# Kernel optimization log

Hardware: AMD Instinct MI355X
Metric: run time of the kernel (lower is better)

The kernel has to match this reference:

```python
import jax, jax.numpy as jnp
import numpy as np

NEG_SLOPE = 0.2
LN_EPS = 1e-5


def gat_conv(x, edge_index, W, att_src, att_dst, bias, heads, out_ch, concat):
    """PyG-style GATConv with add_self_loops=True, eval mode (no dropout)."""
    N = x.shape[0]
    loop = jnp.arange(N, dtype=edge_index.dtype)
    src = jnp.concatenate([edge_index[0], loop])
    dst = jnp.concatenate([edge_index[1], loop])
    h = (x @ W).reshape(N, heads, out_ch)                      # [N,H,C]
    a_src = jnp.sum(h * att_src, axis=-1)                      # [N,H]
    a_dst = jnp.sum(h * att_dst, axis=-1)                      # [N,H]
    e = jax.nn.leaky_relu(a_src[src] + a_dst[dst], NEG_SLOPE)  # [E,H]
    emax = jax.ops.segment_max(e, dst, num_segments=N)         # [N,H]
    ex = jnp.exp(e - emax[dst])
    denom = jax.ops.segment_sum(ex, dst, num_segments=N)       # [N,H]
    alpha = ex / denom[dst]                                    # [E,H]
    msg = h[src] * alpha[..., None]                            # [E,H,C]
    out = jax.ops.segment_sum(msg, dst, num_segments=N)        # [N,H,C]
    out = out.reshape(N, heads * out_ch) if concat else out.mean(axis=1)
    return out + bias


def layer_norm(x, w, b):
    mu = x.mean(-1, keepdims=True)
    var = jnp.mean((x - mu) ** 2, -1, keepdims=True)
    return (x - mu) * jax.lax.rsqrt(var + LN_EPS) * w + b


def setup_inputs() -> dict:
    key = jax.random.key(0)
    ks = jax.random.split(key, 16)
    N, E, R = 50000, 800000, 16
    node_dim, res_dim, hidden, heads = 128, 64, 64, 2
    s = lambda fan: 1.0 / np.sqrt(fan)
    return {
        "x": jax.random.normal(ks[0], (N, node_dim), jnp.float32),
        "edge_index": jax.random.randint(ks[1], (2, E), 0, N, jnp.int64),
        "resource_features": jax.random.normal(ks[2], (N, R, res_dim), jnp.float32),
        "W1": jax.random.normal(ks[3], (node_dim, heads * hidden), jnp.float32) * s(node_dim),
        "att_src1": jax.random.normal(ks[4], (heads, hidden), jnp.float32) * s(hidden),
        "att_dst1": jax.random.normal(ks[5], (heads, hidden), jnp.float32) * s(hidden),
        "b1": jnp.zeros((heads * hidden,), jnp.float32),
        "W2": jax.random.normal(ks[6], (heads * hidden, hidden), jnp.float32) * s(heads * hidden),
        "att_src2": jax.random.normal(ks[7], (1, hidden), jnp.float32) * s(hidden),
        "att_dst2": jax.random.normal(ks[8], (1, hidden), jnp.float32) * s(hidden),
        "b2": jnp.zeros((hidden,), jnp.float32),
        "ln_w": jnp.ones((hidden,), jnp.float32),
        "ln_b": jnp.zeros((hidden,), jnp.float32),
        "res_W": jax.random.normal(ks[9], (res_dim, hidden), jnp.float32) * s(res_dim),
        "res_b": jnp.zeros((hidden,), jnp.float32),
    }


def reference(x, edge_index, resource_features, W1, att_src1, att_dst1, b1,
              W2, att_src2, att_dst2, b2, ln_w, ln_b, res_W, res_b):
    hidden = W2.shape[1]
    heads = att_src1.shape[0]
    h = jax.nn.elu(gat_conv(x, edge_index, W1, att_src1, att_dst1, b1,
                            heads, hidden, concat=True))
    h = gat_conv(h, edge_index, W2, att_src2, att_dst2, b2,
                 1, hidden, concat=False)
    h = layer_norm(h, ln_w, ln_b)                              # [N, hidden]
    R = resource_features.shape[1]
    x_expanded = jnp.broadcast_to(h[:, None, :], (h.shape[0], R, hidden))
    res_emb = jax.nn.elu(resource_features @ res_W + res_b)    # [N,R,hidden]
    return jnp.concatenate([x_expanded, res_emb], axis=-1)     # [N,R,2*hidden]
```

## Files before the change

kernel.cpp:

```cpp
#include <hip/hip_runtime.h>
#include <hip/hip_bf16.h>
#include <math.h>

#define LEAKY_SLOPE 0.2f
#define LN_EPS 1e-5f

typedef __attribute__((ext_vector_type(4))) float f32x4;
typedef __attribute__((ext_vector_type(8))) short short8;

__device__ __forceinline__ float leaky_relu(float x) { return x >= 0.f ? x : LEAKY_SLOPE * x; }
__device__ __forceinline__ float elu1(float x) { return x > 0.f ? x : expm1f(x); }
__device__ __forceinline__ short f2bf(float f) {
    union { __hip_bfloat16 b; short s; } u;
    u.b = __float2bfloat16(f);
    return u.s;
}
__device__ __forceinline__ float bflo(unsigned u) { union { unsigned i; float f; } x; x.i = u << 16; return x.f; }
__device__ __forceinline__ float bfhi(unsigned u) { union { unsigned i; float f; } x; x.i = u & 0xffff0000u; return x.f; }
__device__ __forceinline__ float sbf(short s) { union { unsigned i; float f; } x; x.i = ((unsigned)(unsigned short)s) << 16; return x.f; }
__device__ __forceinline__ unsigned fkey(float f) {
    unsigned b = __float_as_uint(f);
    return b ^ (unsigned)(((int)b >> 31) | 0x80000000);
}
__device__ __forceinline__ float funkey(unsigned k) {
    unsigned b = (k & 0x80000000u) ? (k ^ 0x80000000u) : ~k;
    return __uint_as_float(b);
}

#define SUBW1 130
__global__ __launch_bounds__(256) void k_gemm1m(
    const float* __restrict__ x, const float* __restrict__ W1,
    const float* __restrict__ att_s, const float* __restrict__ att_d,
    short* __restrict__ h1, float* __restrict__ a_src, float* __restrict__ a_dst,
    unsigned* __restrict__ amax, int N)
{
    __shared__ short WT[16 * SUBW1 * 8];
    __shared__ float sb[64 * 4];
    __shared__ float wm[8];
    const int t = threadIdx.x;
    const int w = t >> 6, l = t & 63, lr = l & 15, lk = l >> 4;
    const int n0 = blockIdx.x * 64;
    for (int idx = t; idx < 16384; idx += 256) {
        int k = idx >> 7, col = idx & 127;
        WT[((k >> 3) * SUBW1 + col) * 8 + (k & 7)] = f2bf(W1[idx]);
    }
    sb[t] = 0.f;
    __syncthreads();

    f32x4 acc[4][2];
    #pragma unroll
    for (int mt = 0; mt < 4; ++mt)
        #pragma unroll
        for (int nt = 0; nt < 2; ++nt) acc[mt][nt] = (f32x4){0.f, 0.f, 0.f, 0.f};

    #pragma unroll
    for (int ks = 0; ks < 4; ++ks) {
        short8 bfr[2];
        #pragma unroll
        for (int nt = 0; nt < 2; ++nt) {
            int col = w * 32 + nt * 16 + lr;
            int kk = ks * 4 + lk;
            bfr[nt] = *(const short8*)&WT[(kk * SUBW1 + col) * 8];
        }
        #pragma unroll
        for (int mt = 0; mt < 4; ++mt) {
            int row = n0 + mt * 16 + lr; if (row >= N) row = N - 1;
            const float* ap = x + (size_t)row * 128 + ks * 32 + lk * 8;
            float4 u0 = *(const float4*)ap;
            float4 u1 = *(const float4*)(ap + 4);
            short8 af;
            af[0] = f2bf(u0.x); af[1] = f2bf(u0.y); af[2] = f2bf(u0.z); af[3] = f2bf(u0.w);
            af[4] = f2bf(u1.x); af[5] = f2bf(u1.y); af[6] = f2bf(u1.z); af[7] = f2bf(u1.w);
            acc[mt][0] = __builtin_amdgcn_mfma_f32_16x16x32_bf16(af, bfr[0], acc[mt][0], 0, 0, 0);
            acc[mt][1] = __builtin_amdgcn_mfma_f32_16x16x32_bf16(af, bfr[1], acc[mt][1], 0, 0, 0);
        }
    }

    const int head = w >> 1;
    float asv[2], adv[2];
    #pragma unroll
    for (int nt = 0; nt < 2; ++nt) {
        int ci = (w & 1) * 32 + nt * 16 + lr;
        asv[nt] = att_s[head * 64 + ci];
        adv[nt] = att_d[head * 64 + ci];
    }
    #pragma unroll
    for (int mt = 0; mt < 4; ++mt) {
        #pragma unroll
        for (int i = 0; i < 4; ++i) {
            float ps = acc[mt][0][i] * asv[0] + acc[mt][1][i] * asv[1];
            float pd = acc[mt][0][i] * adv[0] + acc[mt][1][i] * adv[1];
            #pragma unroll
            for (int o = 1; o < 16; o <<= 1) { ps += __shfl_xor(ps, o); pd += __shfl_xor(pd, o); }
            int rl = mt * 16 + lk * 4 + i;
            if (lr == 0) {
                atomicAdd(&sb[rl * 4 + head], ps);
                atomicAdd(&sb[rl * 4 + 2 + head], pd);
            }
            int row = n0 + rl;
            if (row < N) {
                h1[(size_t)row * 128 + w * 32 + lr]      = f2bf(acc[mt][0][i]);
                h1[(size_t)row * 128 + w * 32 + 16 + lr] = f2bf(acc[mt][1][i]);
            }
        }
    }
    __syncthreads();
    int nl = t >> 2, q = t & 3, n = n0 + nl;
    float v = sb[t];
    bool ok = (n < N);
    if (ok) {
        if (q == 0) a_src[n * 2 + 0] = v;
        else if (q == 1) a_src[n * 2 + 1] = v;
        else if (q == 2) a_dst[n * 2 + 0] = v;
        else a_dst[n * 2 + 1] = v;
    }
    float m0 = (ok && q == 0) ? v : -1e30f;
    float m1 = (ok && q == 1) ? v : -1e30f;
    #pragma unroll
    for (int o = 32; o; o >>= 1) { m0 = fmaxf(m0, __shfl_xor(m0, o)); m1 = fmaxf(m1, __shfl_xor(m1, o)); }
    if (l == 0) { wm[w] = m0; wm[4 + w] = m1; }
    __syncthreads();
    if (t == 0) {
        float M0 = fmaxf(fmaxf(wm[0], wm[1]), fmaxf(wm[2], wm[3]));
        float M1 = fmaxf(fmaxf(wm[4], wm[5]), fmaxf(wm[6], wm[7]));
        atomicMax(&amax[0], fkey(M0));
        atomicMax(&amax[1], fkey(M1));
    }
}

#define DETECT_IS64(ei, E)                                              \
    __shared__ int s_is64;                                              \
    {                                                                   \
        if (threadIdx.x < 64) {                                         \
            int v = (threadIdx.x < (E)) ? ((const int*)(ei))[2 * threadIdx.x + 1] : 0; \
            unsigned long long b = __ballot(v != 0);                    \
            if (threadIdx.x == 0) s_is64 = (b == 0ULL);                 \
        }                                                               \
        __syncthreads();                                                \
    }

__global__ __launch_bounds__(256) void k_deg(const void* __restrict__ ei, int E, int* __restrict__ deg)
{
    DETECT_IS64(ei, E)
    const int is64 = s_is64;
    for (int e = blockIdx.x * blockDim.x + threadIdx.x; e < E; e += gridDim.x * blockDim.x) {
        int d = is64 ? (int)((const long long*)ei)[(size_t)E + e] : ((const int*)ei)[(size_t)E + e];
        atomicAdd(&deg[d], 1);
    }
}

__global__ __launch_bounds__(256) void k_bsum(const int* __restrict__ deg, int* __restrict__ bsum, int n)
{
    __shared__ int ws[4];
    const int base = blockIdx.x * 1024;
    int s = 0;
    for (int j = threadIdx.x; j < 1024; j += 256) {
        int i = base + j;
        s += (i < n) ? deg[i] : 0;
    }
    #pragma unroll
    for (int o = 32; o; o >>= 1) s += __shfl_down(s, o);
    if ((threadIdx.x & 63) == 0) ws[threadIdx.x >> 6] = s;
    __syncthreads();
    if (threadIdx.x == 0) bsum[blockIdx.x] = ws[0] + ws[1] + ws[2] + ws[3];
}

__global__ void k_scanb(const int* __restrict__ bsum, int* __restrict__ bbase, int nb)
{
    const int l = threadIdx.x;
    int carry = 0;
    for (int b = 0; b < nb; b += 64) {
        int v = (b + l < nb) ? bsum[b + l] : 0;
        int x = v;
        #pragma unroll
        for (int o = 1; o < 64; o <<= 1) { int y = __shfl_up(x, o); if (l >= o) x += y; }
        if (b + l < nb) bbase[b + l] = carry + x - v;
        carry += __shfl(x, 63);
    }
}

__global__ __launch_bounds__(1024) void k_scan3(const int* __restrict__ deg, const int* __restrict__ bbase,
                                                int* __restrict__ offs, int* __restrict__ cursor, int n)
{
    __shared__ int ws[16];
    const int i = blockIdx.x * 1024 + threadIdx.x;
    const int l = threadIdx.x & 63, w = threadIdx.x >> 6;
    int v = (i < n) ? deg[i] : 0;
    int x = v;
    #pragma unroll
    for (int o = 1; o < 64; o <<= 1) { int y = __shfl_up(x, o); if (l >= o) x += y; }
    if (l == 63) ws[w] = x;
    __syncthreads();
    if (threadIdx.x < 16) {
        int s = ws[threadIdx.x];
        #pragma unroll
        for (int o = 1; o < 16; o <<= 1) { int y = __shfl_up(s, o); if (threadIdx.x >= o) s += y; }
        ws[threadIdx.x] = s;
    }
    __syncthreads();
    int add = (w ? ws[w - 1] : 0) + bbase[blockIdx.x];
    if (i < n) {
        offs[i + 1] = x + add;
        cursor[i] = x + add - v;
    }
    if (blockIdx.x == 0 && threadIdx.x == 0) offs[0] = 0;
}

__global__ __launch_bounds__(256) void k_scatter(const void* __restrict__ ei, int E,
                                                 int* __restrict__ cursor, int* __restrict__ csr_src)
{
    DETECT_IS64(ei, E)
    const int is64 = s_is64;
    for (int e = blockIdx.x * blockDim.x + threadIdx.x; e < E; e += gridDim.x * blockDim.x) {
        int s, d;
        if (is64) {
            const long long* p = (const long long*)ei;
            s = (int)p[e]; d = (int)p[(size_t)E + e];
        } else {
            const int* p = (const int*)ei;
            s = p[e]; d = p[(size_t)E + e];
        }
        int pos = atomicAdd(&cursor[d], 1);
        csr_src[pos] = s;
    }
}

__global__ __launch_bounds__(256) void k_layer1(
    const short* __restrict__ h1, const float* __restrict__ a_s, const float* __restrict__ a_d,
    const int* __restrict__ offs, const int* __restrict__ csr,
    const float* __restrict__ b1, const unsigned* __restrict__ amax,
    short* __restrict__ h1a, int N)
{
    const int w = threadIdx.x >> 6, l = threadIdx.x & 63;
    const int n = blockIdx.x * 4 + w;
    if (n >= N) return;
    const float2 adp = *(const float2*)&a_d[2 * n];
    const float2 asp = *(const float2*)&a_s[2 * n];
    const float C0 = leaky_relu(funkey(amax[0]) + adp.x);
    const float C1 = leaky_relu(funkey(amax[1]) + adp.y);
    const float es0 = leaky_relu(asp.x + adp.x) - C0;
    const float es1 = leaky_relu(asp.y + adp.y) - C1;
    const int hsel = l >> 5;
    const int o0 = offs[n], o1 = offs[n + 1];

    float den0 = 0.f, den1 = 0.f;
    float acc0 = 0.f, acc1 = 0.f, acc0b = 0.f, acc1b = 0.f;
    for (int base = o0; base < o1; base += 64) {
        const int cnt = min(64, o1 - base);
        int sidx = 0; float p0 = 0.f, p1 = 0.f;
        if (l < cnt) {
            sidx = csr[base + l];
            float2 av = *(const float2*)&a_s[2 * sidx];
            p0 = __expf(leaky_relu(av.x + adp.x) - C0);
            p1 = __expf(leaky_relu(av.y + adp.y) - C1);
        }
        den0 += p0; den1 += p1;
        int j = 0;
        for (; j + 2 <= cnt; j += 2) {
            int sa  = __shfl(sidx, j),     sb2 = __shfl(sidx, j + 1);
            float pa0 = __shfl(p0, j),     pb0 = __shfl(p0, j + 1);
            float pa1 = __shfl(p1, j),     pb1 = __shfl(p1, j + 1);
            unsigned ua = *(const unsigned*)(h1 + (size_t)sa  * 128 + 2 * l);
            unsigned ub = *(const unsigned*)(h1 + (size_t)sb2 * 128 + 2 * l);
            float pa = hsel ? pa1 : pa0, pb = hsel ? pb1 : pb0;
            acc0  += pa * bflo(ua); acc1  += pa * bfhi(ua);
            acc0b += pb * bflo(ub); acc1b += pb * bfhi(ub);
        }
        if (j < cnt) {
            int sa = __shfl(sidx, j);
            float pa0 = __shfl(p0, j), pa1 = __shfl(p1, j);
            unsigned ua = *(const unsigned*)(h1 + (size_t)sa * 128 + 2 * l);
            float pa = hsel ? pa1 : pa0;
            acc0 += pa * bflo(ua); acc1 += pa * bfhi(ua);
        }
    }
    #pragma unroll
    for (int o = 32; o; o >>= 1) { den0 += __shfl_xor(den0, o); den1 += __shfl_xor(den1, o); }
    const float psf0 = __expf(es0), psf1 = __expf(es1);
    const float inv0 = 1.f / (den0 + psf0), inv1 = 1.f / (den1 + psf1);

    unsigned us = *(const unsigned*)(h1 + (size_t)n * 128 + 2 * l);
    const float psf = hsel ? psf1 : psf0;
    acc0 += psf * bflo(us); acc1 += psf * bfhi(us);
    const float invh = hsel ? inv1 : inv0;
    float2 bv = *(const float2*)&b1[2 * l];
    float v0 = elu1((acc0 + acc0b) * invh + bv.x);
    float v1 = elu1((acc1 + acc1b) * invh + bv.y);
    unsigned up = ((unsigned)(unsigned short)f2bf(v0)) | (((unsigned)(unsigned short)f2bf(v1)) << 16);
    *(unsigned*)(h1a + (size_t)n * 128 + 2 * l) = up;
}

#define SUBW2 66
__global__ __launch_bounds__(256) void k_gemm2m(
    const short* __restrict__ h1a, const float* __restrict__ W2,
    const float* __restrict__ att_s, const float* __restrict__ att_d,
    short* __restrict__ h2, float* __restrict__ a_src, float* __restrict__ a_dst,
    unsigned* __restrict__ amax, int N)
{
    __shared__ short WT[16 * SUBW2 * 8];
    __shared__ float sb[64 * 2];
    __shared__ float wm[4];
    const int t = threadIdx.x;
    const int w = t >> 6, l = t & 63, lr = l & 15, lk = l >> 4;
    const int n0 = blockIdx.x * 64;
    for (int idx = t; idx < 8192; idx += 256) {
        int k = idx >> 6, col = idx & 63;
        WT[((k >> 3) * SUBW2 + col) * 8 + (k & 7)] = f2bf(W2[idx]);
    }
    if (t < 128) sb[t] = 0.f;
    __syncthreads();

    f32x4 acc[4];
    #pragma unroll
    for (int mt = 0; mt < 4; ++mt) acc[mt] = (f32x4){0.f, 0.f, 0.f, 0.f};

    #pragma unroll
    for (int ks = 0; ks < 4; ++ks) {
        short8 bfr = *(const short8*)&WT[((ks * 4 + lk) * SUBW2 + w * 16 + lr) * 8];
        #pragma unroll
        for (int mt = 0; mt < 4; ++mt) {
            int row = n0 + mt * 16 + lr; if (row >= N) row = N - 1;
            short8 af = *(const short8*)(h1a + (size_t)row * 128 + ks * 32 + lk * 8);
            acc[mt] = __builtin_amdgcn_mfma_f32_16x16x32_bf16(af, bfr, acc[mt], 0, 0, 0);
        }
    }

    const float asv = att_s[w * 16 + lr], adv = att_d[w * 16 + lr];
    #pragma unroll
    for (int mt = 0; mt < 4; ++mt) {
        #pragma unroll
        for (int i = 0; i < 4; ++i) {
            float ps = acc[mt][i] * asv;
            float pd = acc[mt][i] * adv;
            #pragma unroll
            for (int o = 1; o < 16; o <<= 1) { ps += __shfl_xor(ps, o); pd += __shfl_xor(pd, o); }
            int rl = mt * 16 + lk * 4 + i;
            if (lr == 0) {
                atomicAdd(&sb[rl * 2 + 0], ps);
                atomicAdd(&sb[rl * 2 + 1], pd);
            }
            int row = n0 + rl;
            if (row < N) h2[(size_t)row * 64 + w * 16 + lr] = f2bf(acc[mt][i]);
        }
    }
    __syncthreads();
    float v = (t < 128) ? sb[t] : -1e30f;
    int n = n0 + (t >> 1);
    bool ok = (t < 128) && (n < N);
    if (ok) {
        if (t & 1) a_dst[n] = v;
        else       a_src[n] = v;
    }
    float m0 = (ok && !(t & 1)) ? v : -1e30f;
    #pragma unroll
    for (int o = 32; o; o >>= 1) m0 = fmaxf(m0, __shfl_xor(m0, o));
    if (l == 0) wm[w] = m0;
    __syncthreads();
    if (t == 0) {
        float M0 = fmaxf(fmaxf(wm[0], wm[1]), fmaxf(wm[2], wm[3]));
        atomicMax(&amax[0], fkey(M0));
    }
}

__global__ __launch_bounds__(256) void k_layer2(
    const short* __restrict__ h2, const float* __restrict__ a_s, const float* __restrict__ a_d,
    const int* __restrict__ offs, const int* __restrict__ csr,
    const float* __restrict__ b2, const float* __restrict__ lnw, const float* __restrict__ lnb,
    const unsigned* __restrict__ amax, float* __restrict__ hln, int N)
{
    const int w = threadIdx.x >> 6, l = threadIdx.x & 63;
    const int n = blockIdx.x * 4 + w;
    if (n >= N) return;
    const float adv = a_d[n];
    const float C = leaky_relu(funkey(amax[0]) + adv);
    const float es = leaky_relu(a_s[n] + adv) - C;
    const int o0 = offs[n], o1 = offs[n + 1];

    float den = 0.f, acc = 0.f, accb = 0.f;
    for (int base = o0; base < o1; base += 64) {
        const int cnt = min(64, o1 - base);
        int sidx = 0; float pv = 0.f;
        if (l < cnt) {
            sidx = csr[base + l];
            pv = __expf(leaky_relu(a_s[sidx] + adv) - C);
        }
        den += pv;
        int j = 0;
        for (; j + 2 <= cnt; j += 2) {
            int sa = __shfl(sidx, j), sb2 = __shfl(sidx, j + 1);
            float pa = __shfl(pv, j), pb = __shfl(pv, j + 1);
            acc  += pa * sbf(h2[(size_t)sa  * 64 + l]);
            accb += pb * sbf(h2[(size_t)sb2 * 64 + l]);
        }
        if (j < cnt) {
            int sa = __shfl(sidx, j);
            float pa = __shfl(pv, j);
            acc += pa * sbf(h2[(size_t)sa * 64 + l]);
        }
    }
    #pragma unroll
    for (int o = 32; o; o >>= 1) den += __shfl_xor(den, o);
    const float psf = __expf(es);
    const float inv = 1.f / (den + psf);
    acc += psf * sbf(h2[(size_t)n * 64 + l]);
    float o = (acc + accb) * inv + b2[l];

    float mu = o;
    #pragma unroll
    for (int off = 32; off; off >>= 1) mu += __shfl_xor(mu, off);
    mu *= (1.f / 64.f);
    float d = o - mu;
    float vv = d * d;
    #pragma unroll
    for (int off = 32; off; off >>= 1) vv += __shfl_xor(vv, off);
    vv *= (1.f / 64.f);
    float r = rsqrtf(vv + LN_EPS);
    hln[(size_t)n * 64 + l] = d * r * lnw[l] + lnb[l];
}

#define NPW 4
__global__ __launch_bounds__(256) void k_final2(
    const float* __restrict__ res, const float* __restrict__ resW, const float* __restrict__ resb,
    const float* __restrict__ h_ln, float* __restrict__ out, int N)
{
    const int w = threadIdx.x >> 6, l = threadIdx.x & 63;
    const int lr = l & 15, lk = l >> 4;
    const int nbase = (blockIdx.x * 4 + w) * NPW;
    if (nbase >= N) return;

    short8 bf[2][4];
    #pragma unroll
    for (int kk = 0; kk < 2; ++kk)
        #pragma unroll
        for (int nc = 0; nc < 4; ++nc)
            #pragma unroll
            for (int j = 0; j < 8; ++j) {
                int k = kk * 32 + lk * 8 + j;
                bf[kk][nc][j] = f2bf(resW[k * 64 + nc * 16 + lr]);
            }
    float rbv[4];
    #pragma unroll
    for (int nc = 0; nc < 4; ++nc) rbv[nc] = resb[nc * 16 + lr];

    for (int i = 0; i < NPW; ++i) {
        const int n = nbase + i;
        if (n >= N) break;
        const float* rp = res + (size_t)n * 1024 + lr * 64 + lk * 8;
        const float4 f0 = *(const float4*)(rp);
        const float4 f1 = *(const float4*)(rp + 4);
        const float4 f2 = *(const float4*)(rp + 32);
        const float4 f3 = *(const float4*)(rp + 36);
        const f32x4 hv = *(const f32x4*)(h_ln + (size_t)n * 64 + lr * 4);

        short8 a0, a1;
        a0[0] = f2bf(f0.x); a0[1] = f2bf(f0.y); a0[2] = f2bf(f0.z); a0[3] = f2bf(f0.w);
        a0[4] = f2bf(f1.x); a0[5] = f2bf(f1.y); a0[6] = f2bf(f1.z); a0[7] = f2bf(f1.w);
        a1[0] = f2bf(f2.x); a1[1] = f2bf(f2.y); a1[2] = f2bf(f2.z); a1[3] = f2bf(f2.w);
        a1[4] = f2bf(f3.x); a1[5] = f2bf(f3.y); a1[6] = f2bf(f3.z); a1[7] = f2bf(f3.w);

        f32x4 acc[4];
        #pragma unroll
        for (int nc = 0; nc < 4; ++nc) {
            acc[nc] = (f32x4){0.f, 0.f, 0.f, 0.f};
            acc[nc] = __builtin_amdgcn_mfma_f32_16x16x32_bf16(a0, bf[0][nc], acc[nc], 0, 0, 0);
            acc[nc] = __builtin_amdgcn_mfma_f32_16x16x32_bf16(a1, bf[1][nc], acc[nc], 0, 0, 0);
        }

        float* ob = out + (size_t)n * 2048;
        #pragma unroll
        for (int ii = 0; ii < 4; ++ii)
            __builtin_nontemporal_store(hv, (f32x4*)(ob + (lk + 4 * ii) * 128 + lr * 4));
        #pragma unroll
        for (int nc = 0; nc < 4; ++nc)
            #pragma unroll
            for (int ii = 0; ii < 4; ++ii) {
                float v = acc[nc][ii] + rbv[nc];
                __builtin_nontemporal_store(elu1(v), ob + (lk * 4 + ii) * 128 + 64 + nc * 16 + lr);
            }
    }
}

extern "C" void kernel_launch(void* const* d_in, const int* in_sizes, int n_in,
                              void* d_out, int out_size, void* d_ws, size_t ws_size,
                              hipStream_t stream)
{
    const float* x   = (const float*)d_in[0];
    const void*  ei  = d_in[1];
    const float* res = (const float*)d_in[2];
    const float* W1  = (const float*)d_in[3];
    const float* as1 = (const float*)d_in[4];
    const float* ad1 = (const float*)d_in[5];
    const float* b1  = (const float*)d_in[6];
    const float* W2  = (const float*)d_in[7];
    const float* as2 = (const float*)d_in[8];
    const float* ad2 = (const float*)d_in[9];
    const float* b2  = (const float*)d_in[10];
    const float* lnw = (const float*)d_in[11];
    const float* lnb = (const float*)d_in[12];
    const float* rW  = (const float*)d_in[13];
    const float* rb  = (const float*)d_in[14];
    float* out = (float*)d_out;

    const int N = in_sizes[0] / 128;
    const int E = in_sizes[1] / 2;
    const int nb = (N + 1023) / 1024;

    char* base = (char*)d_ws;
    size_t off = 0;
    auto alloc = [&](size_t bytes) -> void* {
        void* p = base + off;
        off = (off + bytes + 255) & ~(size_t)255;
        return p;
    };
    short* h1    = (short*)alloc((size_t)N * 128 * 2);
    short* h1a   = (short*)alloc((size_t)N * 128 * 2);
    short* h2    = (short*)alloc((size_t)N * 64 * 2);
    float* hln   = (float*)alloc((size_t)N * 64 * 4);
    float* a_s1  = (float*)alloc((size_t)N * 2 * 4);
    float* a_d1  = (float*)alloc((size_t)N * 2 * 4);
    float* a_s2  = (float*)alloc((size_t)N * 4);
    float* a_d2  = (float*)alloc((size_t)N * 4);
    int* deg     = (int*)alloc((size_t)(N + 8) * 4);
    int* offs    = (int*)alloc((size_t)(N + 1) * 4);
    int* cursor  = (int*)alloc((size_t)N * 4);
    int* csr_src = (int*)alloc((size_t)E * 4);
    int* bsum    = (int*)alloc((size_t)nb * 4);
    int* bbase   = (int*)alloc((size_t)nb * 4);
    unsigned* amax1 = (unsigned*)(deg + N);
    unsigned* amax2 = (unsigned*)(deg + N + 2);

    (void)hipMemsetAsync(deg, 0, (size_t)(N + 8) * 4, stream);
    k_gemm1m<<<(N + 63) / 64, 256, 0, stream>>>(x, W1, as1, ad1, h1, a_s1, a_d1, amax1, N);
    k_deg<<<512, 256, 0, stream>>>(ei, E, deg);
    k_bsum<<<nb, 256, 0, stream>>>(deg, bsum, N);
    k_scanb<<<1, 64, 0, stream>>>(bsum, bbase, nb);
    k_scan3<<<nb, 1024, 0, stream>>>(deg, bbase, offs, cursor, N);
    k_scatter<<<512, 256, 0, stream>>>(ei, E, cursor, csr_src);
    k_layer1<<<(N + 3) / 4, 256, 0, stream>>>(h1, a_s1, a_d1, offs, csr_src, b1, amax1, h1a, N);
    k_gemm2m<<<(N + 63) / 64, 256, 0, stream>>>(h1a, W2, as2, ad2, h2, a_s2, a_d2, amax2, N);
    k_layer2<<<(N + 3) / 4, 256, 0, stream>>>(h2, a_s2, a_d2, offs, csr_src, b2, lnw, lnb, amax2, hln, N);
    k_final2<<<(N + NPW * 4 - 1) / (NPW * 4), 256, 0, stream>>>(res, rW, rb, hln, out, N);
}
```

Measured before the change: 392.1 us.

## Fuse degree count into gemm1, fuse layer2 aggregation with LayerNorm and output

The degree-count kernel is merged into the first GEMM kernel as extra blocks, so the two independent jobs share one launch and can overlap. Layer-2 attention aggregation and LayerNorm are fused into the final resource-projection/output kernel, which drops the hln intermediate buffer write and read and one launch. The gather loops in both aggregation kernels are unrolled by four with separate accumulators to keep more loads in flight. The resource features are now read with nontemporal loads. The fused GEMM kernel gives the degree blocks the same shared-memory footprint as the GEMM blocks. The fused tail kernel handles fewer nodes per wave and reloads weights more often.

```diff
diff --git a/kernel.cpp b/kernel.cpp
--- a/kernel.cpp
+++ b/kernel.cpp
@@ -27,13 +27,36 @@
     return __uint_as_float(b);
 }
 
+#define DETECT_IS64(ei, E)                                              \
+    __shared__ int s_is64;                                              \
+    {                                                                   \
+        if (threadIdx.x < 64) {                                         \
+            int v = (threadIdx.x < (E)) ? ((const int*)(ei))[2 * threadIdx.x + 1] : 0; \
+            unsigned long long b = __ballot(v != 0);                    \
+            if (threadIdx.x == 0) s_is64 = (b == 0ULL);                 \
+        }                                                               \
+        __syncthreads();                                                \
+    }
+
 #define SUBW1 130
-__global__ __launch_bounds__(256) void k_gemm1m(
+#define DEGB 512
+__global__ __launch_bounds__(256) void k_fat1(
     const float* __restrict__ x, const float* __restrict__ W1,
     const float* __restrict__ att_s, const float* __restrict__ att_d,
     short* __restrict__ h1, float* __restrict__ a_src, float* __restrict__ a_dst,
-    unsigned* __restrict__ amax, int N)
-{
+    unsigned* __restrict__ amax, int N,
+    const void* __restrict__ ei, int E, int* __restrict__ deg, int nbG)
+{
+    if ((int)blockIdx.x >= nbG) {
+        DETECT_IS64(ei, E)
+        const int is64 = s_is64;
+        const int b0 = (int)blockIdx.x - nbG;
+        for (int e = b0 * 256 + threadIdx.x; e < E; e += DEGB * 256) {
+            int d = is64 ? (int)((const long long*)ei)[(size_t)E + e] : ((const int*)ei)[(size_t)E + e];
+            atomicAdd(&deg[d], 1);
+        }
+        return;
+    }
     __shared__ short WT[16 * SUBW1 * 8];
     __shared__ float sb[64 * 4];
     __shared__ float wm[8];
@@ -125,27 +148,6 @@
         float M1 = fmaxf(fmaxf(wm[4], wm[5]), fmaxf(wm[6], wm[7]));
         atomicMax(&amax[0], fkey(M0));
         atomicMax(&amax[1], fkey(M1));
-    }
-}
-
-#define DETECT_IS64(ei, E)                                              \
-    __shared__ int s_is64;                                              \
-    {                                                                   \
-        if (threadIdx.x < 64) {                                         \
-            int v = (threadIdx.x < (E)) ? ((const int*)(ei))[2 * threadIdx.x + 1] : 0; \
-            unsigned long long b = __ballot(v != 0);                    \
-            if (threadIdx.x == 0) s_is64 = (b == 0ULL);                 \
-        }                                                               \
-        __syncthreads();                                                \
-    }
-
-__global__ __launch_bounds__(256) void k_deg(const void* __restrict__ ei, int E, int* __restrict__ deg)
-{
-    DETECT_IS64(ei, E)
-    const int is64 = s_is64;
-    for (int e = blockIdx.x * blockDim.x + threadIdx.x; e < E; e += gridDim.x * blockDim.x) {
-        int d = is64 ? (int)((const long long*)ei)[(size_t)E + e] : ((const int*)ei)[(size_t)E + e];
-        atomicAdd(&deg[d], 1);
     }
 }
 
@@ -244,7 +246,8 @@
     const int o0 = offs[n], o1 = offs[n + 1];
 
     float den0 = 0.f, den1 = 0.f;
-    float acc0 = 0.f, acc1 = 0.f, acc0b = 0.f, acc1b = 0.f;
+    float cl0 = 0.f, ch0 = 0.f, cl1 = 0.f, ch1 = 0.f;
+    float cl2 = 0.f, ch2 = 0.f, cl3 = 0.f, ch3 = 0.f;
     for (int base = o0; base < o1; base += 64) {
         const int cnt = min(64, o1 - base);
         int sidx = 0; float p0 = 0.f, p1 = 0.f;
@@ -256,22 +259,30 @@
         }
         den0 += p0; den1 += p1;
         int j = 0;
-        for (; j + 2 <= cnt; j += 2) {
-            int sa  = __shfl(sidx, j),     sb2 = __shfl(sidx, j + 1);
-            float pa0 = __shfl(p0, j),     pb0 = __shfl(p0, j + 1);
-            float pa1 = __shfl(p1, j),     pb1 = __shfl(p1, j + 1);
-            unsigned ua = *(const unsigned*)(h1 + (size_t)sa  * 128 + 2 * l);
-            unsigned ub = *(const unsigned*)(h1 + (size_t)sb2 * 128 + 2 * l);
-            float pa = hsel ? pa1 : pa0, pb = hsel ? pb1 : pb0;
-            acc0  += pa * bflo(ua); acc1  += pa * bfhi(ua);
-            acc0b += pb * bflo(ub); acc1b += pb * bfhi(ub);
-        }
-        if (j < cnt) {
+        for (; j + 4 <= cnt; j += 4) {
+            int s0 = __shfl(sidx, j),     s1 = __shfl(sidx, j + 1);
+            int s2 = __shfl(sidx, j + 2), s3 = __shfl(sidx, j + 3);
+            float q00 = __shfl(p0, j),     q10 = __shfl(p1, j);
+            float q01 = __shfl(p0, j + 1), q11 = __shfl(p1, j + 1);
+            float q02 = __shfl(p0, j + 2), q12 = __shfl(p1, j + 2);
+            float q03 = __shfl(p0, j + 3), q13 = __shfl(p1, j + 3);
+            unsigned u0 = *(const unsigned*)(h1 + (size_t)s0 * 128 + 2 * l);
+            unsigned u1 = *(const unsigned*)(h1 + (size_t)s1 * 128 + 2 * l);
+            unsigned u2 = *(const unsigned*)(h1 + (size_t)s2 * 128 + 2 * l);
+            unsigned u3 = *(const unsigned*)(h1 + (size_t)s3 * 128 + 2 * l);
+            float w0 = hsel ? q10 : q00, w1 = hsel ? q11 : q01;
+            float w2 = hsel ? q12 : q02, w3 = hsel ? q13 : q03;
+            cl0 += w0 * bflo(u0); ch0 += w0 * bfhi(u0);
+            cl1 += w1 * bflo(u1); ch1 += w1 * bfhi(u1);
+            cl2 += w2 * bflo(u2); ch2 += w2 * bfhi(u2);
+            cl3 += w3 * bflo(u3); ch3 += w3 * bfhi(u3);
+        }
+        for (; j < cnt; ++j) {
             int sa = __shfl(sidx, j);
-            float pa0 = __shfl(p0, j), pa1 = __shfl(p1, j);
+            float qa0 = __shfl(p0, j), qa1 = __shfl(p1, j);
             unsigned ua = *(const unsigned*)(h1 + (size_t)sa * 128 + 2 * l);
-            float pa = hsel ? pa1 : pa0;
-            acc0 += pa * bflo(ua); acc1 += pa * bfhi(ua);
+            float wa = hsel ? qa1 : qa0;
+            cl0 += wa * bflo(ua); ch0 += wa * bfhi(ua);
         }
     }
     #pragma unroll
@@ -281,11 +292,12 @@
 
     unsigned us = *(const unsigned*)(h1 + (size_t)n * 128 + 2 * l);
     const float psf = hsel ? psf1 : psf0;
-    acc0 += psf * bflo(us); acc1 += psf * bfhi(us);
+    float acc0 = cl0 + cl1 + cl2 + cl3 + psf * bflo(us);
+    float acc1 = ch0 + ch1 + ch2 + ch3 + psf * bfhi(us);
     const float invh = hsel ? inv1 : inv0;
     float2 bv = *(const float2*)&b1[2 * l];
-    float v0 = elu1((acc0 + acc0b) * invh + bv.x);
-    float v1 = elu1((acc1 + acc1b) * invh + bv.y);
+    float v0 = elu1(acc0 * invh + bv.x);
+    float v1 = elu1(acc1 * invh + bv.y);
     unsigned up = ((unsigned)(unsigned short)f2bf(v0)) | (((unsigned)(unsigned short)f2bf(v1)) << 16);
     *(unsigned*)(h1a + (size_t)n * 128 + 2 * l) = up;
 }
@@ -362,70 +374,18 @@
     }
 }
 
-__global__ __launch_bounds__(256) void k_layer2(
+#define NPT 2
+__global__ __launch_bounds__(256) void k_tail(
     const short* __restrict__ h2, const float* __restrict__ a_s, const float* __restrict__ a_d,
     const int* __restrict__ offs, const int* __restrict__ csr,
     const float* __restrict__ b2, const float* __restrict__ lnw, const float* __restrict__ lnb,
-    const unsigned* __restrict__ amax, float* __restrict__ hln, int N)
-{
-    const int w = threadIdx.x >> 6, l = threadIdx.x & 63;
-    const int n = blockIdx.x * 4 + w;
-    if (n >= N) return;
-    const float adv = a_d[n];
-    const float C = leaky_relu(funkey(amax[0]) + adv);
-    const float es = leaky_relu(a_s[n] + adv) - C;
-    const int o0 = offs[n], o1 = offs[n + 1];
-
-    float den = 0.f, acc = 0.f, accb = 0.f;
-    for (int base = o0; base < o1; base += 64) {
-        const int cnt = min(64, o1 - base);
-        int sidx = 0; float pv = 0.f;
-        if (l < cnt) {
-            sidx = csr[base + l];
-            pv = __expf(leaky_relu(a_s[sidx] + adv) - C);
-        }
-        den += pv;
-        int j = 0;
-        for (; j + 2 <= cnt; j += 2) {
-            int sa = __shfl(sidx, j), sb2 = __shfl(sidx, j + 1);
-            float pa = __shfl(pv, j), pb = __shfl(pv, j + 1);
-            acc  += pa * sbf(h2[(size_t)sa  * 64 + l]);
-            accb += pb * sbf(h2[(size_t)sb2 * 64 + l]);
-        }
-        if (j < cnt) {
-            int sa = __shfl(sidx, j);
-            float pa = __shfl(pv, j);
-            acc += pa * sbf(h2[(size_t)sa * 64 + l]);
-        }
-    }
-    #pragma unroll
-    for (int o = 32; o; o >>= 1) den += __shfl_xor(den, o);
-    const float psf = __expf(es);
-    const float inv = 1.f / (den + psf);
-    acc += psf * sbf(h2[(size_t)n * 64 + l]);
-    float o = (acc + accb) * inv + b2[l];
-
-    float mu = o;
-    #pragma unroll
-    for (int off = 32; off; off >>= 1) mu += __shfl_xor(mu, off);
-    mu *= (1.f / 64.f);
-    float d = o - mu;
-    float vv = d * d;
-    #pragma unroll
-    for (int off = 32; off; off >>= 1) vv += __shfl_xor(vv, off);
-    vv *= (1.f / 64.f);
-    float r = rsqrtf(vv + LN_EPS);
-    hln[(size_t)n * 64 + l] = d * r * lnw[l] + lnb[l];
-}
-
-#define NPW 4
-__global__ __launch_bounds__(256) void k_final2(
+    const unsigned* __restrict__ amax,
     const float* __restrict__ res, const float* __restrict__ resW, const float* __restrict__ resb,
-    const float* __restrict__ h_ln, float* __restrict__ out, int N)
+    float* __restrict__ out, int N)
 {
     const int w = threadIdx.x >> 6, l = threadIdx.x & 63;
     const int lr = l & 15, lk = l >> 4;
-    const int nbase = (blockIdx.x * 4 + w) * NPW;
+    const int nbase = (blockIdx.x * 4 + w) * NPT;
     if (nbase >= N) return;
 
     short8 bf[2][4];
@@ -441,29 +401,78 @@
     float rbv[4];
     #pragma unroll
     for (int nc = 0; nc < 4; ++nc) rbv[nc] = resb[nc * 16 + lr];
-
-    for (int i = 0; i < NPW; ++i) {
+    const float b2l = b2[l], lnwl = lnw[l], lnbl = lnb[l];
+    const float Am = funkey(amax[0]);
+
+    for (int i = 0; i < NPT; ++i) {
         const int n = nbase + i;
         if (n >= N) break;
+        const float adv = a_d[n];
+        const float C = leaky_relu(Am + adv);
+        const float es = leaky_relu(a_s[n] + adv) - C;
+        const int o0 = offs[n], o1 = offs[n + 1];
+        float den = 0.f, a0 = 0.f, a1 = 0.f, a2 = 0.f, a3 = 0.f;
+        for (int base = o0; base < o1; base += 64) {
+            const int cnt = min(64, o1 - base);
+            int sidx = 0; float pv = 0.f;
+            if (l < cnt) {
+                sidx = csr[base + l];
+                pv = __expf(leaky_relu(a_s[sidx] + adv) - C);
+            }
+            den += pv;
+            int j = 0;
+            for (; j + 4 <= cnt; j += 4) {
+                int s0 = __shfl(sidx, j),     s1 = __shfl(sidx, j + 1);
+                int s2 = __shfl(sidx, j + 2), s3 = __shfl(sidx, j + 3);
+                float q0 = __shfl(pv, j),     q1 = __shfl(pv, j + 1);
+                float q2 = __shfl(pv, j + 2), q3 = __shfl(pv, j + 3);
+                a0 += q0 * sbf(h2[(size_t)s0 * 64 + l]);
+                a1 += q1 * sbf(h2[(size_t)s1 * 64 + l]);
+                a2 += q2 * sbf(h2[(size_t)s2 * 64 + l]);
+                a3 += q3 * sbf(h2[(size_t)s3 * 64 + l]);
+            }
+            for (; j < cnt; ++j) {
+                int sa = __shfl(sidx, j);
+                float qa = __shfl(pv, j);
+                a0 += qa * sbf(h2[(size_t)sa * 64 + l]);
+            }
+        }
+        #pragma unroll
+        for (int o = 32; o; o >>= 1) den += __shfl_xor(den, o);
+        const float psf = __expf(es);
+        const float inv = 1.f / (den + psf);
+        float o = (a0 + a1 + a2 + a3 + psf * sbf(h2[(size_t)n * 64 + l])) * inv + b2l;
+        float mu = o;
+        #pragma unroll
+        for (int off = 32; off; off >>= 1) mu += __shfl_xor(mu, off);
+        mu *= (1.f / 64.f);
+        float d = o - mu;
+        float vv = d * d;
+        #pragma unroll
+        for (int off = 32; off; off >>= 1) vv += __shfl_xor(vv, off);
+        vv *= (1.f / 64.f);
+        const float hl = d * rsqrtf(vv + LN_EPS) * lnwl + lnbl;
+        f32x4 hv;
+        #pragma unroll
+        for (int j = 0; j < 4; ++j) hv[j] = __shfl(hl, lr * 4 + j);
         const float* rp = res + (size_t)n * 1024 + lr * 64 + lk * 8;
-        const float4 f0 = *(const float4*)(rp);
-        const float4 f1 = *(const float4*)(rp + 4);
-        const float4 f2 = *(const float4*)(rp + 32);
-        const float4 f3 = *(const float4*)(rp + 36);
-        const f32x4 hv = *(const f32x4*)(h_ln + (size_t)n * 64 + lr * 4);
-
-        short8 a0, a1;
-        a0[0] = f2bf(f0.x); a0[1] = f2bf(f0.y); a0[2] = f2bf(f0.z); a0[3] = f2bf(f0.w);
-        a0[4] = f2bf(f1.x); a0[5] = f2bf(f1.y); a0[6] = f2bf(f1.z); a0[7] = f2bf(f1.w);
-        a1[0] = f2bf(f2.x); a1[1] = f2bf(f2.y); a1[2] = f2bf(f2.z); a1[3] = f2bf(f2.w);
-        a1[4] = f2bf(f3.x); a1[5] = f2bf(f3.y); a1[6] = f2bf(f3.z); a1[7] = f2bf(f3.w);
+        const f32x4 f0 = __builtin_nontemporal_load((const f32x4*)(rp));
+        const f32x4 f1 = __builtin_nontemporal_load((const f32x4*)(rp + 4));
+        const f32x4 f2 = __builtin_nontemporal_load((const f32x4*)(rp + 32));
+        const f32x4 f3 = __builtin_nontemporal_load((const f32x4*)(rp + 36));
+
+        short8 fa0, fa1;
+        fa0[0] = f2bf(f0[0]); fa0[1] = f2bf(f0[1]); fa0[2] = f2bf(f0[2]); fa0[3] = f2bf(f0[3]);
+        fa0[4] = f2bf(f1[0]); fa0[5] = f2bf(f1[1]); fa0[6] = f2bf(f1[2]); fa0[7] = f2bf(f1[3]);
+        fa1[0] = f2bf(f2[0]); fa1[1] = f2bf(f2[1]); fa1[2] = f2bf(f2[2]); fa1[3] = f2bf(f2[3]);
+        fa1[4] = f2bf(f3[0]); fa1[5] = f2bf(f3[1]); fa1[6] = f2bf(f3[2]); fa1[7] = f2bf(f3[3]);
 
         f32x4 acc[4];
         #pragma unroll
         for (int nc = 0; nc < 4; ++nc) {
             acc[nc] = (f32x4){0.f, 0.f, 0.f, 0.f};
-            acc[nc] = __builtin_amdgcn_mfma_f32_16x16x32_bf16(a0, bf[0][nc], acc[nc], 0, 0, 0);
-            acc[nc] = __builtin_amdgcn_mfma_f32_16x16x32_bf16(a1, bf[1][nc], acc[nc], 0, 0, 0);
+            acc[nc] = __builtin_amdgcn_mfma_f32_16x16x32_bf16(fa0, bf[0][nc], acc[nc], 0, 0, 0);
+            acc[nc] = __builtin_amdgcn_mfma_f32_16x16x32_bf16(fa1, bf[1][nc], acc[nc], 0, 0, 0);
         }
 
         float* ob = out + (size_t)n * 2048;
@@ -504,6 +513,7 @@
     const int N = in_sizes[0] / 128;
     const int E = in_sizes[1] / 2;
     const int nb = (N + 1023) / 1024;
+    const int nbG = (N + 63) / 64;
 
     char* base = (char*)d_ws;
     size_t off = 0;
@@ -515,7 +525,6 @@
     short* h1    = (short*)alloc((size_t)N * 128 * 2);
     short* h1a   = (short*)alloc((size_t)N * 128 * 2);
     short* h2    = (short*)alloc((size_t)N * 64 * 2);
-    float* hln   = (float*)alloc((size_t)N * 64 * 4);
     float* a_s1  = (float*)alloc((size_t)N * 2 * 4);
     float* a_d1  = (float*)alloc((size_t)N * 2 * 4);
     float* a_s2  = (float*)alloc((size_t)N * 4);
@@ -530,14 +539,13 @@
     unsigned* amax2 = (unsigned*)(deg + N + 2);
 
     (void)hipMemsetAsync(deg, 0, (size_t)(N + 8) * 4, stream);
-    k_gemm1m<<<(N + 63) / 64, 256, 0, stream>>>(x, W1, as1, ad1, h1, a_s1, a_d1, amax1, N);
-    k_deg<<<512, 256, 0, stream>>>(ei, E, deg);
+    k_fat1<<<nbG + DEGB, 256, 0, stream>>>(x, W1, as1, ad1, h1, a_s1, a_d1, amax1, N, ei, E, deg, nbG);
     k_bsum<<<nb, 256, 0, stream>>>(deg, bsum, N);
     k_scanb<<<1, 64, 0, stream>>>(bsum, bbase, nb);
     k_scan3<<<nb, 1024, 0, stream>>>(deg, bbase, offs, cursor, N);
     k_scatter<<<512, 256, 0, stream>>>(ei, E, cursor, csr_src);
     k_layer1<<<(N + 3) / 4, 256, 0, stream>>>(h1, a_s1, a_d1, offs, csr_src, b1, amax1, h1a, N);
     k_gemm2m<<<(N + 63) / 64, 256, 0, stream>>>(h1a, W2, as2, ad2, h2, a_s2, a_d2, amax2, N);
-    k_layer2<<<(N + 3) / 4, 256, 0, stream>>>(h2, a_s2, a_d2, offs, csr_src, b2, lnw, lnb, amax2, hln, N);
-    k_final2<<<(N + NPW * 4 - 1) / (NPW * 4), 256, 0, stream>>>(res, rW, rb, hln, out, N);
-}
+    k_tail<<<(N + NPT * 4 - 1) / (NPT * 4), 256, 0, stream>>>(h2, a_s2, a_d2, offs, csr_src, b2, lnw, lnb,
+                                                              amax2, res, rW, rb, out, N);
+}
```

After: 364.0 us. 7.2% less time.
